# Kernel optimization log

Measured on AMD Instinct MI355X. Metric: run time of the kernel, lower is better.

Reference implementation:

```python
import jax, jax.numpy as jnp
import numpy as np

N, E, D, L, G, C = 20000, 320000, 512, 6, 64, 10
EPS = 1e-5


def setup_inputs() -> dict:
    key = jax.random.key(0)
    ks = jax.random.split(key, 8)
    s = 0.05  # small init scale to keep activations sane across 6 layers
    x = jax.random.normal(ks[0], (N, D), jnp.float32)
    edge_index = jax.random.randint(ks[1], (2, E), 0, N, jnp.int32)
    batch = jnp.sort(jax.random.randint(ks[2], (N,), 0, G, jnp.int32))
    W_rel = jax.random.normal(ks[3], (L, D, D), jnp.float32) * s
    b_rel = jnp.zeros((L, D), jnp.float32)
    W_root = jax.random.normal(ks[4], (L, D, D), jnp.float32) * s
    gamma = jnp.ones((L, D), jnp.float32)
    beta = jnp.zeros((L, D), jnp.float32)
    lin_w = jax.random.normal(ks[5], (D, C), jnp.float32) * s
    lin_b = jnp.zeros((C,), jnp.float32)
    return {"x": x, "edge_index": edge_index, "batch": batch,
            "W_rel": W_rel, "b_rel": b_rel, "W_root": W_root,
            "gamma": gamma, "beta": beta, "lin_w": lin_w, "lin_b": lin_b}


def reference(x, edge_index, batch, W_rel, b_rel, W_root, gamma, beta, lin_w, lin_b):
    # PyG GraphConv (aggr='add'): out = segment_sum(x[src] -> dst) @ W_rel + b_rel + x @ W_root
    src, dst = edge_index[0], edge_index[1]
    n = x.shape[0]
    for l in range(W_rel.shape[0]):  # 6 structurally identical layers
        agg = jax.ops.segment_sum(x[src], dst, num_segments=n)  # [N, D]
        h = agg @ W_rel[l] + b_rel[l] + x @ W_root[l]
        # BatchNorm1d in training mode: biased batch statistics over nodes
        mu = jnp.mean(h, axis=0)
        var = jnp.mean(jnp.square(h - mu), axis=0)
        x = jax.nn.relu((h - mu) * jax.lax.rsqrt(var + EPS) * gamma[l] + beta[l])
    # global_mean_pool over per-node graph ids
    sums = jax.ops.segment_sum(x, batch, num_segments=G)              # [G, D]
    counts = jax.ops.segment_sum(jnp.ones((n,), x.dtype), batch, num_segments=G)
    pooled = sums / jnp.maximum(counts, 1.0)[:, None]
    return pooled @ lin_w + lin_b  # [G, C]
```

## Files before the change

kernel.cpp:

```cpp
#include <hip/hip_runtime.h>


typedef unsigned short u16;
typedef unsigned int u32;
typedef __attribute__((ext_vector_type(8))) short bf16x8;
typedef __attribute__((ext_vector_type(16))) float f32x16;

#define DFEAT 512
#define KDIM 1024
#define NLAYER 6
#define NGRAPH 64
#define NCLS 10
#define BN_EPS 1e-5f

__device__ __forceinline__ float bf_lo(u32 u) { union { u32 i; float f; } v; v.i = u << 16; return v.f; }
__device__ __forceinline__ float bf_hi(u32 u) { union { u32 i; float f; } v; v.i = u & 0xFFFF0000u; return v.f; }
__device__ __forceinline__ u16 f2bf(float f) {
  union { float f; u32 i; } v; v.f = f;
  u32 r = v.i + 0x7FFFu + ((v.i >> 16) & 1u);
  return (u16)(r >> 16);
}
__device__ __forceinline__ u32 pack2(float lo, float hi) {
  return (u32)f2bf(lo) | ((u32)f2bf(hi) << 16);
}

__device__ __forceinline__ void gload_lds16(const u16* g, u16* lds_base) {
  __builtin_amdgcn_global_load_lds(
      (const __attribute__((address_space(1))) u32*)g,
      (__attribute__((address_space(3))) u32*)lds_base, 16, 0, 0);
}

__global__ void prep_kernel(const int* __restrict__ ei, int* __restrict__ counts, int E,
                            const float* __restrict__ Wrel, const float* __restrict__ Wroot,
                            u16* __restrict__ Wt,
                            const float* __restrict__ x, u16* __restrict__ A, int M,
                            int histB, int wB) {
  int b = blockIdx.x;
  if (b < histB) {
    int e = b * 256 + threadIdx.x;
    if (e < E) atomicAdd(&counts[ei[E + e]], 1);
  } else if (b < histB + wB) {
    int idx = (b - histB) * 256 + threadIdx.x;
    int k = idx & 1023;
    int n = (idx >> 10) & 511;
    int l = idx >> 19;
    float v = (k < DFEAT) ? Wrel[((size_t)l * DFEAT + k) * DFEAT + n]
                          : Wroot[((size_t)l * DFEAT + (k - DFEAT)) * DFEAT + n];
    Wt[idx] = f2bf(v);
  } else {
    int idx = (b - histB - wB) * 256 + threadIdx.x;
    int row = idx >> 7;
    int c4 = (idx & 127) * 4;
    if (row < M) {
      float4 v = *(const float4*)&x[(size_t)row * DFEAT + c4];
      uint2 o; o.x = pack2(v.x, v.y); o.y = pack2(v.z, v.w);
      *(uint2*)&A[(size_t)row * KDIM + DFEAT + c4] = o;
    }
  }
}

#define SCHUNK 20
__global__ __launch_bounds__(1024) void scan_kernel(const int* __restrict__ counts,
                                                    int* __restrict__ row_ptr,
                                                    int* __restrict__ cursor, int n) {
  __shared__ int part[1024];
  int tid = threadIdx.x;
  int base = tid * SCHUNK;
  int loc[SCHUNK];
  int s = 0;
#pragma unroll
  for (int i = 0; i < SCHUNK; i++) {
    int idx = base + i;
    int v = (idx < n) ? counts[idx] : 0;
    loc[i] = s; s += v;
  }
  part[tid] = s;
  __syncthreads();
  int x = s;
  for (int off = 1; off < 1024; off <<= 1) {
    int t = (tid >= off) ? part[tid - off] : 0;
    __syncthreads();
    x += t;
    part[tid] = x;
    __syncthreads();
  }
  int offset = x - s;
#pragma unroll
  for (int i = 0; i < SCHUNK; i++) {
    int idx = base + i;
    if (idx < n) { int v = offset + loc[i]; row_ptr[idx] = v; cursor[idx] = v; }
  }
  if (tid == 1023) row_ptr[n] = offset + s;
}

__global__ void scatter_kernel(const int* __restrict__ ei, int* __restrict__ cursor,
                               int* __restrict__ csr_src, int E) {
  int e = blockIdx.x * 256 + threadIdx.x;
  if (e < E) {
    int d = ei[E + e];
    int pos = atomicAdd(&cursor[d], 1);
    csr_src[pos] = ei[e];
  }
}

__device__ __forceinline__ void add8(uint4 v, float2* a) {
  a[0] += make_float2(bf_lo(v.x), bf_hi(v.x));
  a[1] += make_float2(bf_lo(v.y), bf_hi(v.y));
  a[2] += make_float2(bf_lo(v.z), bf_hi(v.z));
  a[3] += make_float2(bf_lo(v.w), bf_hi(v.w));
}

#define GCAP 1536
__global__ __launch_bounds__(256) void gather_kernel(u16* __restrict__ A,
                                                     const int* __restrict__ row_ptr,
                                                     const int* __restrict__ csr_src, int n) {
  __shared__ int sidx[GCAP];
  int b = blockIdx.x;
  int slice = b & 7;
  int grp = b >> 3;
  int tid = threadIdx.x;
  int r0 = grp * 32;
  int rend = (r0 + 32 < n) ? (r0 + 32) : n;
  int wbeg = row_ptr[r0], wend = row_ptr[rend];
  int cnt = wend - wbeg;
  bool lds_ok = (cnt <= GCAP);
  if (lds_ok)
    for (int t = tid; t < cnt; t += 256) sidx[t] = csr_src[wbeg + t];
  __syncthreads();

  int wid = tid >> 6, lane = tid & 63;
  int dsub = lane >> 3, fl = lane & 7;
  int dst = r0 + wid * 8 + dsub;
  if (dst >= n) return;
  int cc = slice * 64 + fl * 8;
  const u16* Sx = A + DFEAT + cc;
  int db = row_ptr[dst], de = row_ptr[dst + 1];
  float2 a[4] = {};
  if (lds_ok) {
    int e = db - wbeg, ee = de - wbeg;
    for (; e + 7 < ee; e += 8) {
      int s0 = sidx[e + 0], s1 = sidx[e + 1], s2 = sidx[e + 2], s3 = sidx[e + 3];
      int s4 = sidx[e + 4], s5 = sidx[e + 5], s6 = sidx[e + 6], s7 = sidx[e + 7];
      uint4 v0 = *(const uint4*)&Sx[(size_t)s0 * KDIM];
      uint4 v1 = *(const uint4*)&Sx[(size_t)s1 * KDIM];
      uint4 v2 = *(const uint4*)&Sx[(size_t)s2 * KDIM];
      uint4 v3 = *(const uint4*)&Sx[(size_t)s3 * KDIM];
      uint4 v4 = *(const uint4*)&Sx[(size_t)s4 * KDIM];
      uint4 v5 = *(const uint4*)&Sx[(size_t)s5 * KDIM];
      uint4 v6 = *(const uint4*)&Sx[(size_t)s6 * KDIM];
      uint4 v7 = *(const uint4*)&Sx[(size_t)s7 * KDIM];
      add8(v0, a); add8(v1, a); add8(v2, a); add8(v3, a);
      add8(v4, a); add8(v5, a); add8(v6, a); add8(v7, a);
    }
    for (; e < ee; ++e) {
      uint4 v = *(const uint4*)&Sx[(size_t)sidx[e] * KDIM];
      add8(v, a);
    }
  } else {
    for (int e = db; e < de; ++e) {
      uint4 v = *(const uint4*)&Sx[(size_t)csr_src[e] * KDIM];
      add8(v, a);
    }
  }
  uint4 o;
  o.x = pack2(a[0].x, a[0].y); o.y = pack2(a[1].x, a[1].y);
  o.z = pack2(a[2].x, a[2].y); o.w = pack2(a[3].x, a[3].y);
  *(uint4*)&A[(size_t)dst * KDIM + cc] = o;
}

#define BM 128
#define BN 128
#define BK 64
#define CSTR 132
__global__ __launch_bounds__(256, 4) void gemm_kernel(const u16* __restrict__ A,
                                                      const u16* __restrict__ Bt,
                                                      const float* __restrict__ bias,
                                                      u16* __restrict__ Hb,
                                                      float* __restrict__ sums, int M) {
  const int lin = blockIdx.x;
  const int bx = ((lin >> 5) << 3) + (lin & 7);
  const int by = (lin >> 3) & 3;
  const int m0 = bx * BM;
  if (m0 >= M) return;
  const int n0 = by * BN;

  __shared__ u16 smem[BM * CSTR];
  __shared__ float sred[2 * BN];
  u16* As = smem;
  u16* Bs = smem + BM * BK;
  const int tid = threadIdx.x;
  const int wid = tid >> 6, lane = tid & 63;
  const int wm = wid >> 1, wn = wid & 1;
  const int l31 = lane & 31, half = lane >> 5;

  if (tid < 2 * BN) sred[tid] = 0.f;

  const int dr = lane >> 3;
  const int gcol = ((lane & 7) ^ dr) * 8;
  int arow[4], brow[4];
#pragma unroll
  for (int t = 0; t < 4; t++) {
    int r = wid * 32 + t * 8 + dr;
    int ar = m0 + r; if (ar >= M) ar = M - 1;
    arow[t] = ar;
    brow[t] = n0 + r;
  }

  f32x16 acc[2][2] = {};

  for (int k0 = 0; k0 < KDIM; k0 += BK) {
    __syncthreads();
#pragma unroll
    for (int t = 0; t < 4; t++)
      gload_lds16(&A[(size_t)arow[t] * KDIM + k0 + gcol], &As[(wid * 32 + t * 8) * BK]);
#pragma unroll
    for (int t = 0; t < 4; t++)
      gload_lds16(&Bt[(size_t)brow[t] * KDIM + k0 + gcol], &Bs[(wid * 32 + t * 8) * BK]);
    __syncthreads();
#pragma unroll
    for (int ks = 0; ks < 4; ks++) {
      int slot = ((ks * 2 + half) ^ (l31 & 7)) * 8;
      bf16x8 a0 = *(const bf16x8*)&As[(wm * 64 + l31) * BK + slot];
      bf16x8 a1 = *(const bf16x8*)&As[(wm * 64 + 32 + l31) * BK + slot];
      bf16x8 b0 = *(const bf16x8*)&Bs[(wn * 64 + l31) * BK + slot];
      bf16x8 b1 = *(const bf16x8*)&Bs[(wn * 64 + 32 + l31) * BK + slot];
      acc[0][0] = __builtin_amdgcn_mfma_f32_32x32x16_bf16(a0, b0, acc[0][0], 0, 0, 0);
      acc[0][1] = __builtin_amdgcn_mfma_f32_32x32x16_bf16(a0, b1, acc[0][1], 0, 0, 0);
      acc[1][0] = __builtin_amdgcn_mfma_f32_32x32x16_bf16(a1, b0, acc[1][0], 0, 0, 0);
      acc[1][1] = __builtin_amdgcn_mfma_f32_32x32x16_bf16(a1, b1, acc[1][1], 0, 0, 0);
    }
  }

  __syncthreads();

#pragma unroll
  for (int nt = 0; nt < 2; nt++) {
    int colt = wn * 64 + nt * 32 + l31;
    float bv = bias[n0 + colt];
    float s = 0.f, s2 = 0.f;
#pragma unroll
    for (int mt = 0; mt < 2; mt++) {
      int rbase = wm * 64 + mt * 32 + half * 4;
#pragma unroll
      for (int reg = 0; reg < 16; reg++) {
        int rowt = rbase + (reg & 3) + 8 * (reg >> 2);
        float v = acc[mt][nt][reg] + bv;
        smem[rowt * CSTR + colt] = f2bf(v);
        if (m0 + rowt < M) { s += v; s2 += v * v; }
      }
    }
    s  += __shfl_xor(s, 32);
    s2 += __shfl_xor(s2, 32);
    if (half == 0) {
      atomicAdd(&sred[colt], s);
      atomicAdd(&sred[BN + colt], s2);
    }
  }
  __syncthreads();

  const int rsub = tid >> 4;
  const int c8 = (tid & 15) * 8;
#pragma unroll
  for (int it = 0; it < 8; it++) {
    int rowt = it * 16 + rsub;
    int grow = m0 + rowt;
    if (grow < M) {
      uint4 v = *(const uint4*)&smem[rowt * CSTR + c8];
      *(uint4*)&Hb[(size_t)grow * DFEAT + n0 + c8] = v;
    }
  }
  if (tid < BN) {
    atomicAdd(&sums[n0 + tid], sred[tid]);
    atomicAdd(&sums[DFEAT + n0 + tid], sred[BN + tid]);
  }
}

__global__ void norm_kernel(const u16* __restrict__ Hb, const float* __restrict__ sums,
                            const float* __restrict__ gamma, const float* __restrict__ beta,
                            u16* __restrict__ A, int M, float invN) {
  int idx = blockIdx.x * 256 + threadIdx.x;
  int row = idx >> 6;
  int c8 = (idx & 63) * 8;
  if (row >= M) return;
  float sc[8], sh[8];
#pragma unroll
  for (int j = 0; j < 8; j++) {
    int c = c8 + j;
    float mu = sums[c] * invN;
    float var = sums[DFEAT + c] * invN - mu * mu;
    float s = gamma[c] * rsqrtf(var + BN_EPS);
    sc[j] = s;
    sh[j] = beta[c] - mu * s;
  }
  uint4 h = *(const uint4*)&Hb[(size_t)row * DFEAT + c8];
  float x0 = fmaxf(bf_lo(h.x) * sc[0] + sh[0], 0.f);
  float x1 = fmaxf(bf_hi(h.x) * sc[1] + sh[1], 0.f);
  float x2 = fmaxf(bf_lo(h.y) * sc[2] + sh[2], 0.f);
  float x3 = fmaxf(bf_hi(h.y) * sc[3] + sh[3], 0.f);
  float x4 = fmaxf(bf_lo(h.z) * sc[4] + sh[4], 0.f);
  float x5 = fmaxf(bf_hi(h.z) * sc[5] + sh[5], 0.f);
  float x6 = fmaxf(bf_lo(h.w) * sc[6] + sh[6], 0.f);
  float x7 = fmaxf(bf_hi(h.w) * sc[7] + sh[7], 0.f);
  uint4 o; o.x = pack2(x0, x1); o.y = pack2(x2, x3);
  o.z = pack2(x4, x5); o.w = pack2(x6, x7);
  *(uint4*)&A[(size_t)row * KDIM + DFEAT + c8] = o;
}

__device__ __forceinline__ int lower_bound_dev(const int* a, int n, int v) {
  int lo = 0, hi = n;
  while (lo < hi) { int mid = (lo + hi) >> 1; if (a[mid] < v) lo = mid + 1; else hi = mid; }
  return lo;
}

__global__ __launch_bounds__(1024) void pool_kernel(const u16* __restrict__ Hb,
                                                    const float* __restrict__ sums,
                                                    const float* __restrict__ gamma,
                                                    const float* __restrict__ beta,
                                                    const int* __restrict__ batch,
                                                    float* __restrict__ pooled, int n, float invN) {
  __shared__ float red[DFEAT];
  int g = blockIdx.x;
  int tid = threadIdx.x;
  if (tid < DFEAT) red[tid] = 0.f;
  int lo = lower_bound_dev(batch, n, g);
  int hi = lower_bound_dev(batch, n, g + 1);
  int rowOff = tid >> 6, lane = tid & 63;
  int c0 = lane * 8;
  float sc[8], sh[8];
#pragma unroll
  for (int j = 0; j < 8; j++) {
    int c = c0 + j;
    float mu = sums[c] * invN;
    float var = sums[DFEAT + c] * invN - mu * mu;
    float s = gamma[c] * rsqrtf(var + BN_EPS);
    sc[j] = s;
    sh[j] = beta[c] - mu * s;
  }
  float a[8] = {};
  for (int r = lo + rowOff; r < hi; r += 16) {
    uint4 v = *(const uint4*)&Hb[(size_t)r * DFEAT + c0];
    float e0 = bf_lo(v.x), e1 = bf_hi(v.x), e2 = bf_lo(v.y), e3 = bf_hi(v.y);
    float e4 = bf_lo(v.z), e5 = bf_hi(v.z), e6 = bf_lo(v.w), e7 = bf_hi(v.w);
    a[0] += fmaxf(e0 * sc[0] + sh[0], 0.f); a[1] += fmaxf(e1 * sc[1] + sh[1], 0.f);
    a[2] += fmaxf(e2 * sc[2] + sh[2], 0.f); a[3] += fmaxf(e3 * sc[3] + sh[3], 0.f);
    a[4] += fmaxf(e4 * sc[4] + sh[4], 0.f); a[5] += fmaxf(e5 * sc[5] + sh[5], 0.f);
    a[6] += fmaxf(e6 * sc[6] + sh[6], 0.f); a[7] += fmaxf(e7 * sc[7] + sh[7], 0.f);
  }
  __syncthreads();
#pragma unroll
  for (int j = 0; j < 8; j++) atomicAdd(&red[c0 + j], a[j]);
  __syncthreads();
  if (tid < DFEAT) pooled[g * DFEAT + tid] = red[tid] / fmaxf((float)(hi - lo), 1.0f);
}

__global__ __launch_bounds__(64) void final_kernel(const float* __restrict__ pooled,
                                                   const float* __restrict__ lin_w,
                                                   const float* __restrict__ lin_b,
                                                   float* __restrict__ out) {
  int g = blockIdx.x;
  int lane = threadIdx.x;
  float acc[NCLS] = {};
  float4 p0 = *(const float4*)&pooled[g * DFEAT + lane * 8];
  float4 p1 = *(const float4*)&pooled[g * DFEAT + lane * 8 + 4];
  float pv[8] = {p0.x, p0.y, p0.z, p0.w, p1.x, p1.y, p1.z, p1.w};
#pragma unroll
  for (int j = 0; j < 8; j++) {
    int k = lane * 8 + j;
#pragma unroll
    for (int c = 0; c < NCLS; c++) acc[c] += pv[j] * lin_w[k * NCLS + c];
  }
#pragma unroll
  for (int off = 32; off > 0; off >>= 1)
#pragma unroll
    for (int c = 0; c < NCLS; c++) acc[c] += __shfl_down(acc[c], off);
  if (lane == 0)
#pragma unroll
    for (int c = 0; c < NCLS; c++) out[g * NCLS + c] = acc[c] + lin_b[c];
}

extern "C" void kernel_launch(void* const* d_in, const int* in_sizes, int n_in,
                              void* d_out, int out_size, void* d_ws, size_t ws_size,
                              hipStream_t stream) {
  const float* x      = (const float*)d_in[0];
  const int*   ei     = (const int*)d_in[1];
  const int*   batch  = (const int*)d_in[2];
  const float* W_rel  = (const float*)d_in[3];
  const float* b_rel  = (const float*)d_in[4];
  const float* W_root = (const float*)d_in[5];
  const float* gamma  = (const float*)d_in[6];
  const float* beta   = (const float*)d_in[7];
  const float* lin_w  = (const float*)d_in[8];
  const float* lin_b  = (const float*)d_in[9];
  float* out = (float*)d_out;

  const int N = in_sizes[0] / DFEAT;
  const int E = in_sizes[1] / 2;

  char* p = (char*)d_ws;
  u16*   A       = (u16*)p;    p += (size_t)N * KDIM * 2;
  u16*   Hb      = (u16*)p;    p += (size_t)N * DFEAT * 2;
  u16*   Wt      = (u16*)p;    p += (size_t)NLAYER * DFEAT * KDIM * 2;
  int*   row_ptr = (int*)p;    p += ((size_t)(N + 1) * 4 + 15) / 16 * 16;
  int*   cursor  = (int*)p;    p += (size_t)N * 4;
  int*   csr_src = (int*)p;    p += (size_t)E * 4;
  float* sums    = (float*)p;  p += (size_t)NLAYER * 2 * DFEAT * 4;
  float* pooled  = (float*)p;  p += (size_t)NGRAPH * DFEAT * 4;

  const float invN = 1.0f / (float)N;

  hipMemsetAsync(cursor, 0, (size_t)N * 4, stream);
  hipMemsetAsync(sums, 0, (size_t)NLAYER * 2 * DFEAT * 4, stream);

  const int histB = (E + 255) / 256;
  const int wB = (NLAYER * DFEAT * KDIM) / 256;
  const int xB = (N * 128 + 255) / 256;
  prep_kernel<<<histB + wB + xB, 256, 0, stream>>>(ei, cursor, E, W_rel, W_root, Wt,
                                                   x, A, N, histB, wB);
  scan_kernel<<<1, 1024, 0, stream>>>(cursor, row_ptr, cursor, N);
  scatter_kernel<<<(E + 255) / 256, 256, 0, stream>>>(ei, cursor, csr_src, E);

  const int ngrp8 = ((N + 31) / 32) * 8;
  const int gtiles = (((N + BM - 1) / BM + 7) / 8) * 8 * 4;

  for (int l = 0; l < NLAYER; ++l) {
    float* sums_l = sums + (size_t)l * 2 * DFEAT;
    gather_kernel<<<ngrp8, 256, 0, stream>>>(A, row_ptr, csr_src, N);
    gemm_kernel<<<gtiles, 256, 0, stream>>>(A, Wt + (size_t)l * DFEAT * KDIM,
                                            b_rel + (size_t)l * DFEAT, Hb, sums_l, N);
    if (l < NLAYER - 1)
      norm_kernel<<<(N * 64 + 255) / 256, 256, 0, stream>>>(
          Hb, sums_l, gamma + (size_t)l * DFEAT, beta + (size_t)l * DFEAT, A, N, invN);
  }

  pool_kernel<<<NGRAPH, 1024, 0, stream>>>(Hb, sums + (size_t)(NLAYER - 1) * 2 * DFEAT,
                                           gamma + (size_t)(NLAYER - 1) * DFEAT,
                                           beta + (size_t)(NLAYER - 1) * DFEAT,
                                           batch, pooled, N, invN);
  final_kernel<<<NGRAPH, 64, 0, stream>>>(pooled, lin_w, lin_b, out);
}
```

Before: 601.4 us.

## Fuse BatchNorm+ReLU into next layer's gather and tile the weight transpose

Removes the separate norm kernel. The gather kernel for layers 1 and up now reads raw pre-norm activations from Hb and applies BN scale/shift and ReLU to each gathered neighbor row, while also writing the normalized self row into A. Separately, the weight transpose/convert in prep is restructured to use a 64x64 LDS tile so both the reads and the bf16 writes are coalesced. The fusion saves one full read and write pass of activations per layer and 5 launches. In exchange it adds per-edge FMA and max work and reads denser 512-stride rows from Hb.

```diff
diff --git a/kernel.cpp b/kernel.cpp
--- a/kernel.cpp
+++ b/kernel.cpp
@@ -35,20 +35,45 @@
                             u16* __restrict__ Wt,
                             const float* __restrict__ x, u16* __restrict__ A, int M,
                             int histB, int wB) {
+  __shared__ float tile[64][65];
   int b = blockIdx.x;
+  int tid = threadIdx.x;
   if (b < histB) {
-    int e = b * 256 + threadIdx.x;
+    int e = b * 256 + tid;
     if (e < E) atomicAdd(&counts[ei[E + e]], 1);
   } else if (b < histB + wB) {
-    int idx = (b - histB) * 256 + threadIdx.x;
-    int k = idx & 1023;
-    int n = (idx >> 10) & 511;
-    int l = idx >> 19;
-    float v = (k < DFEAT) ? Wrel[((size_t)l * DFEAT + k) * DFEAT + n]
-                          : Wroot[((size_t)l * DFEAT + (k - DFEAT)) * DFEAT + n];
-    Wt[idx] = f2bf(v);
+    int t = b - histB;
+    int l = t >> 7;
+    int tt = t & 127;
+    int k0 = (tt >> 3) << 6;
+    int n0 = (tt & 7) << 6;
+    int rr = tid >> 4;
+    int c4 = (tid & 15) << 2;
+#pragma unroll
+    for (int i = 0; i < 4; i++) {
+      int k = k0 + i * 16 + rr;
+      const float* src = (k < DFEAT)
+          ? &Wrel[((size_t)l * DFEAT + k) * DFEAT + n0 + c4]
+          : &Wroot[((size_t)l * DFEAT + (k - DFEAT)) * DFEAT + n0 + c4];
+      float4 v = *(const float4*)src;
+      float* d = &tile[i * 16 + rr][c4];
+      d[0] = v.x; d[1] = v.y; d[2] = v.z; d[3] = v.w;
+    }
+    __syncthreads();
+    int nr = tid >> 3;
+    int kc = (tid & 7) << 3;
+#pragma unroll
+    for (int i = 0; i < 2; i++) {
+      int nl = i * 32 + nr;
+      uint4 o;
+      o.x = pack2(tile[kc + 0][nl], tile[kc + 1][nl]);
+      o.y = pack2(tile[kc + 2][nl], tile[kc + 3][nl]);
+      o.z = pack2(tile[kc + 4][nl], tile[kc + 5][nl]);
+      o.w = pack2(tile[kc + 6][nl], tile[kc + 7][nl]);
+      *(uint4*)&Wt[(size_t)(l * DFEAT + n0 + nl) * KDIM + k0 + kc] = o;
+    }
   } else {
-    int idx = (b - histB - wB) * 256 + threadIdx.x;
+    int idx = (b - histB - wB) * 256 + tid;
     int row = idx >> 7;
     int c4 = (idx & 127) * 4;
     if (row < M) {
@@ -103,17 +128,35 @@
   }
 }
 
-__device__ __forceinline__ void add8(uint4 v, float2* a) {
-  a[0] += make_float2(bf_lo(v.x), bf_hi(v.x));
-  a[1] += make_float2(bf_lo(v.y), bf_hi(v.y));
-  a[2] += make_float2(bf_lo(v.z), bf_hi(v.z));
-  a[3] += make_float2(bf_lo(v.w), bf_hi(v.w));
+template <bool FUSED>
+__device__ __forceinline__ void acc8(uint4 v, const float* sc, const float* sh, float2* a) {
+  if constexpr (FUSED) {
+    a[0].x += fmaxf(bf_lo(v.x) * sc[0] + sh[0], 0.f);
+    a[0].y += fmaxf(bf_hi(v.x) * sc[1] + sh[1], 0.f);
+    a[1].x += fmaxf(bf_lo(v.y) * sc[2] + sh[2], 0.f);
+    a[1].y += fmaxf(bf_hi(v.y) * sc[3] + sh[3], 0.f);
+    a[2].x += fmaxf(bf_lo(v.z) * sc[4] + sh[4], 0.f);
+    a[2].y += fmaxf(bf_hi(v.z) * sc[5] + sh[5], 0.f);
+    a[3].x += fmaxf(bf_lo(v.w) * sc[6] + sh[6], 0.f);
+    a[3].y += fmaxf(bf_hi(v.w) * sc[7] + sh[7], 0.f);
+  } else {
+    a[0] += make_float2(bf_lo(v.x), bf_hi(v.x));
+    a[1] += make_float2(bf_lo(v.y), bf_hi(v.y));
+    a[2] += make_float2(bf_lo(v.z), bf_hi(v.z));
+    a[3] += make_float2(bf_lo(v.w), bf_hi(v.w));
+  }
 }
 
 #define GCAP 1536
+template <bool FUSED>
 __global__ __launch_bounds__(256) void gather_kernel(u16* __restrict__ A,
+                                                     const u16* __restrict__ Hb,
+                                                     const float* __restrict__ sums,
+                                                     const float* __restrict__ gamma,
+                                                     const float* __restrict__ beta,
                                                      const int* __restrict__ row_ptr,
-                                                     const int* __restrict__ csr_src, int n) {
+                                                     const int* __restrict__ csr_src,
+                                                     int n, float invN) {
   __shared__ int sidx[GCAP];
   int b = blockIdx.x;
   int slice = b & 7;
@@ -133,7 +176,27 @@
   int dst = r0 + wid * 8 + dsub;
   if (dst >= n) return;
   int cc = slice * 64 + fl * 8;
-  const u16* Sx = A + DFEAT + cc;
+  float sc[8], sh[8];
+  if constexpr (FUSED) {
+#pragma unroll
+    for (int j = 0; j < 8; j++) {
+      int c = cc + j;
+      float mu = sums[c] * invN;
+      float var = sums[DFEAT + c] * invN - mu * mu;
+      float s = gamma[c] * rsqrtf(var + BN_EPS);
+      sc[j] = s;
+      sh[j] = beta[c] - mu * s;
+    }
+    uint4 h = *(const uint4*)&Hb[(size_t)dst * DFEAT + cc];
+    uint4 o;
+    o.x = pack2(fmaxf(bf_lo(h.x) * sc[0] + sh[0], 0.f), fmaxf(bf_hi(h.x) * sc[1] + sh[1], 0.f));
+    o.y = pack2(fmaxf(bf_lo(h.y) * sc[2] + sh[2], 0.f), fmaxf(bf_hi(h.y) * sc[3] + sh[3], 0.f));
+    o.z = pack2(fmaxf(bf_lo(h.z) * sc[4] + sh[4], 0.f), fmaxf(bf_hi(h.z) * sc[5] + sh[5], 0.f));
+    o.w = pack2(fmaxf(bf_lo(h.w) * sc[6] + sh[6], 0.f), fmaxf(bf_hi(h.w) * sc[7] + sh[7], 0.f));
+    *(uint4*)&A[(size_t)dst * KDIM + DFEAT + cc] = o;
+  }
+  const u16* Sx = FUSED ? (Hb + cc) : (A + DFEAT + cc);
+  const size_t RS = FUSED ? DFEAT : KDIM;
   int db = row_ptr[dst], de = row_ptr[dst + 1];
   float2 a[4] = {};
   if (lds_ok) {
@@ -141,25 +204,27 @@
     for (; e + 7 < ee; e += 8) {
       int s0 = sidx[e + 0], s1 = sidx[e + 1], s2 = sidx[e + 2], s3 = sidx[e + 3];
       int s4 = sidx[e + 4], s5 = sidx[e + 5], s6 = sidx[e + 6], s7 = sidx[e + 7];
-      uint4 v0 = *(const uint4*)&Sx[(size_t)s0 * KDIM];
-      uint4 v1 = *(const uint4*)&Sx[(size_t)s1 * KDIM];
-      uint4 v2 = *(const uint4*)&Sx[(size_t)s2 * KDIM];
-      uint4 v3 = *(const uint4*)&Sx[(size_t)s3 * KDIM];
-      uint4 v4 = *(const uint4*)&Sx[(size_t)s4 * KDIM];
-      uint4 v5 = *(const uint4*)&Sx[(size_t)s5 * KDIM];
-      uint4 v6 = *(const uint4*)&Sx[(size_t)s6 * KDIM];
-      uint4 v7 = *(const uint4*)&Sx[(size_t)s7 * KDIM];
-      add8(v0, a); add8(v1, a); add8(v2, a); add8(v3, a);
-      add8(v4, a); add8(v5, a); add8(v6, a); add8(v7, a);
+      uint4 v0 = *(const uint4*)&Sx[(size_t)s0 * RS];
+      uint4 v1 = *(const uint4*)&Sx[(size_t)s1 * RS];
+      uint4 v2 = *(const uint4*)&Sx[(size_t)s2 * RS];
+      uint4 v3 = *(const uint4*)&Sx[(size_t)s3 * RS];
+      uint4 v4 = *(const uint4*)&Sx[(size_t)s4 * RS];
+      uint4 v5 = *(const uint4*)&Sx[(size_t)s5 * RS];
+      uint4 v6 = *(const uint4*)&Sx[(size_t)s6 * RS];
+      uint4 v7 = *(const uint4*)&Sx[(size_t)s7 * RS];
+      acc8<FUSED>(v0, sc, sh, a); acc8<FUSED>(v1, sc, sh, a);
+      acc8<FUSED>(v2, sc, sh, a); acc8<FUSED>(v3, sc, sh, a);
+      acc8<FUSED>(v4, sc, sh, a); acc8<FUSED>(v5, sc, sh, a);
+      acc8<FUSED>(v6, sc, sh, a); acc8<FUSED>(v7, sc, sh, a);
     }
     for (; e < ee; ++e) {
-      uint4 v = *(const uint4*)&Sx[(size_t)sidx[e] * KDIM];
-      add8(v, a);
+      uint4 v = *(const uint4*)&Sx[(size_t)sidx[e] * RS];
+      acc8<FUSED>(v, sc, sh, a);
     }
   } else {
     for (int e = db; e < de; ++e) {
-      uint4 v = *(const uint4*)&Sx[(size_t)csr_src[e] * KDIM];
-      add8(v, a);
+      uint4 v = *(const uint4*)&Sx[(size_t)csr_src[e] * RS];
+      acc8<FUSED>(v, sc, sh, a);
     }
   }
   uint4 o;
@@ -275,37 +340,6 @@
   }
 }
 
-__global__ void norm_kernel(const u16* __restrict__ Hb, const float* __restrict__ sums,
-                            const float* __restrict__ gamma, const float* __restrict__ beta,
-                            u16* __restrict__ A, int M, float invN) {
-  int idx = blockIdx.x * 256 + threadIdx.x;
-  int row = idx >> 6;
-  int c8 = (idx & 63) * 8;
-  if (row >= M) return;
-  float sc[8], sh[8];
-#pragma unroll
-  for (int j = 0; j < 8; j++) {
-    int c = c8 + j;
-    float mu = sums[c] * invN;
-    float var = sums[DFEAT + c] * invN - mu * mu;
-    float s = gamma[c] * rsqrtf(var + BN_EPS);
-    sc[j] = s;
-    sh[j] = beta[c] - mu * s;
-  }
-  uint4 h = *(const uint4*)&Hb[(size_t)row * DFEAT + c8];
-  float x0 = fmaxf(bf_lo(h.x) * sc[0] + sh[0], 0.f);
-  float x1 = fmaxf(bf_hi(h.x) * sc[1] + sh[1], 0.f);
-  float x2 = fmaxf(bf_lo(h.y) * sc[2] + sh[2], 0.f);
-  float x3 = fmaxf(bf_hi(h.y) * sc[3] + sh[3], 0.f);
-  float x4 = fmaxf(bf_lo(h.z) * sc[4] + sh[4], 0.f);
-  float x5 = fmaxf(bf_hi(h.z) * sc[5] + sh[5], 0.f);
-  float x6 = fmaxf(bf_lo(h.w) * sc[6] + sh[6], 0.f);
-  float x7 = fmaxf(bf_hi(h.w) * sc[7] + sh[7], 0.f);
-  uint4 o; o.x = pack2(x0, x1); o.y = pack2(x2, x3);
-  o.z = pack2(x4, x5); o.w = pack2(x6, x7);
-  *(uint4*)&A[(size_t)row * KDIM + DFEAT + c8] = o;
-}
-
 __device__ __forceinline__ int lower_bound_dev(const int* a, int n, int v) {
   int lo = 0, hi = n;
   while (lo < hi) { int mid = (lo + hi) >> 1; if (a[mid] < v) lo = mid + 1; else hi = mid; }
@@ -412,7 +446,7 @@
   hipMemsetAsync(sums, 0, (size_t)NLAYER * 2 * DFEAT * 4, stream);
 
   const int histB = (E + 255) / 256;
-  const int wB = (NLAYER * DFEAT * KDIM) / 256;
+  const int wB = NLAYER * 128;
   const int xB = (N * 128 + 255) / 256;
   prep_kernel<<<histB + wB + xB, 256, 0, stream>>>(ei, cursor, E, W_rel, W_root, Wt,
                                                    x, A, N, histB, wB);
@@ -424,12 +458,16 @@
 
   for (int l = 0; l < NLAYER; ++l) {
     float* sums_l = sums + (size_t)l * 2 * DFEAT;
-    gather_kernel<<<ngrp8, 256, 0, stream>>>(A, row_ptr, csr_src, N);
+    if (l == 0)
+      gather_kernel<false><<<ngrp8, 256, 0, stream>>>(A, Hb, nullptr, nullptr, nullptr,
+                                                      row_ptr, csr_src, N, invN);
+    else
+      gather_kernel<true><<<ngrp8, 256, 0, stream>>>(A, Hb,
+          sums + (size_t)(l - 1) * 2 * DFEAT,
+          gamma + (size_t)(l - 1) * DFEAT, beta + (size_t)(l - 1) * DFEAT,
+          row_ptr, csr_src, N, invN);
     gemm_kernel<<<gtiles, 256, 0, stream>>>(A, Wt + (size_t)l * DFEAT * KDIM,
                                             b_rel + (size_t)l * DFEAT, Hb, sums_l, N);
-    if (l < NLAYER - 1)
-      norm_kernel<<<(N * 64 + 255) / 256, 256, 0, stream>>>(
-          Hb, sums_l, gamma + (size_t)l * DFEAT, beta + (size_t)l * DFEAT, A, N, invN);
   }
 
   pool_kernel<<<NGRAPH, 1024, 0, stream>>>(Hb, sums + (size_t)(NLAYER - 1) * 2 * DFEAT,
```

Result: slower. 625.1 us (+4.0%).
